# Kernel optimization log

Measured on AMD Instinct MI355X. Metric: run time of the kernel, lower is better.

The kernel has to match this reference:

```python
import jax, jax.numpy as jnp
import numpy as np
import math

B, S, D, H = 2, 2048, 1024, 16
DK = D // H

def setup_inputs() -> dict:
    key = jax.random.key(0)
    ks = jax.random.split(key, 12)
    def xavier(k, shape):
        fan_in, fan_out = shape[1], shape[0]
        limit = math.sqrt(6.0 / (fan_in + fan_out))
        return jax.random.uniform(k, shape, jnp.float32, -limit, limit)
    inp = {
        'query': jax.random.normal(ks[0], (B, S, D), jnp.float32),
        'key':   jax.random.normal(ks[1], (B, S, D), jnp.float32),
        'value': jax.random.normal(ks[2], (B, S, D), jnp.float32),
        # causal mask, broadcast over heads: (B, 1, S, S), 1 = keep, 0 = mask
        'mask':  jnp.broadcast_to(jnp.tril(jnp.ones((S, S), jnp.int32)), (B, 1, S, S)),
        'Wq': xavier(ks[3], (D, D)), 'bq': jnp.zeros((D,), jnp.float32),
        'Wk': xavier(ks[4], (D, D)), 'bk': jnp.zeros((D,), jnp.float32),
        'Wv': xavier(ks[5], (D, D)), 'bv': jnp.zeros((D,), jnp.float32),
        'Wo': xavier(ks[6], (D, D)), 'bo': jnp.zeros((D,), jnp.float32),
    }
    return inp

def _split_heads(x):
    # (B, S, D) -> (B, H, S, DK)
    b, s, _ = x.shape
    return x.reshape(b, s, H, DK).transpose(0, 2, 1, 3)

def reference(query, key, value, mask, Wq, bq, Wk, bk, Wv, bv, Wo, bo):
    # torch nn.Linear: y = x @ W.T + b
    Q = _split_heads(query @ Wq.T + bq)   # (B,H,S,DK)
    K = _split_heads(key   @ Wk.T + bk)
    V = _split_heads(value @ Wv.T + bv)
    scores = jnp.einsum('bhqd,bhkd->bhqk', Q, K) / math.sqrt(DK)  # (B,H,S,S)
    scores = jnp.where(mask == 0, jnp.float32(-1e9), scores)
    attn = jax.nn.softmax(scores, axis=-1)  # dropout p=0 -> identity
    out = jnp.einsum('bhqk,bhkd->bhqd', attn, V)  # (B,H,S,DK)
    out = out.transpose(0, 2, 1, 3).reshape(query.shape[0], query.shape[1], D)
    return out @ Wo.T + bo
```

## Files before the change

### kernel.cpp

```cpp
#include <hip/hip_runtime.h>
#include <hip/hip_bf16.h>
#include <type_traits>


typedef __attribute__((ext_vector_type(8))) short short8;
typedef __attribute__((ext_vector_type(4))) short s16x4;
typedef __attribute__((ext_vector_type(4))) float floatx4;

__device__ __forceinline__ short f2bf(float x) {
    union { float f; unsigned u; } v; v.f = x;
    unsigned r = v.u + 0x7fffu + ((v.u >> 16) & 1u);
    return (short)(r >> 16);
}

__device__ __forceinline__ unsigned pk2bf(float a, float b) {
    union { __hip_bfloat162 h2; unsigned u; } cv;
    cv.h2 = __float22bfloat162_rn(make_float2(a, b));
    return cv.u;
}

__device__ __forceinline__ float fast_exp2(float x) {
#if __has_builtin(__builtin_amdgcn_exp2f)
    return __builtin_amdgcn_exp2f(x);
#else
    return __expf(x * 0.69314718056f);
#endif
}

typedef __attribute__((address_space(3))) short lds_short;
typedef __attribute__((address_space(1))) const short glb_short;
__device__ __forceinline__ void load_lds16(const void* g, void* l) {
    __builtin_amdgcn_global_load_lds((glb_short*)g, (lds_short*)l, 16, 0, 0);
}

__global__ __launch_bounds__(256) void cvt_all(
        const float* __restrict__ q, const float* __restrict__ k,
        const float* __restrict__ v,
        const float* __restrict__ wq, const float* __restrict__ wk,
        const float* __restrict__ wv, const float* __restrict__ wo,
        unsigned short* __restrict__ xq, unsigned short* __restrict__ xk,
        unsigned short* __restrict__ xv,
        unsigned short* __restrict__ wqb, unsigned short* __restrict__ wkb,
        unsigned short* __restrict__ wvb, unsigned short* __restrict__ wob) {
    const float* s; unsigned short* d;
    int bx = blockIdx.x;
    switch (blockIdx.y) {
        case 0: s = q; d = xq; break;
        case 1: s = k; d = xk; break;
        case 2: s = v; d = xv; break;
        default: {
            int wsel = bx >> 9; bx &= 511;
            s = (wsel == 0) ? wq : (wsel == 1) ? wk : (wsel == 2) ? wv : wo;
            d = (wsel == 0) ? wqb : (wsel == 1) ? wkb : (wsel == 2) ? wvb : wob;
        }
    }
    size_t i = ((size_t)bx * 256 + threadIdx.x) * 8;
    floatx4 a = *(const floatx4*)(s + i), b2 = *(const floatx4*)(s + i + 4);
    union { unsigned u[4]; short8 v8; } o;
    o.u[0] = pk2bf(a[0], a[1]);  o.u[1] = pk2bf(a[2], a[3]);
    o.u[2] = pk2bf(b2[0], b2[1]); o.u[3] = pk2bf(b2[2], b2[3]);
    *(short8*)(d + i) = o.v8;
}

__global__ __launch_bounds__(256) void gemm_qkv(
        const unsigned short* __restrict__ Xq, const unsigned short* __restrict__ Xk,
        const unsigned short* __restrict__ Xv,
        const unsigned short* __restrict__ Wq, const unsigned short* __restrict__ Wk,
        const unsigned short* __restrict__ Wv,
        const float* __restrict__ bq, const float* __restrict__ bk,
        const float* __restrict__ bv,
        unsigned short* __restrict__ Qb, unsigned short* __restrict__ Kb,
        unsigned short* __restrict__ Vb) {
    constexpr int K = 1024, N = 1024;
    __shared__ short As[128 * 64];
    __shared__ short Bs[128 * 64];
    const int t = threadIdx.x;
    const int slot = blockIdx.x;
    const int p = (slot & 7) + 8 * (slot >> 6);
    const int nx = (slot >> 3) & 7;
    const int chunk = p >> 5, my = p & 31;
    const unsigned short* A = chunk == 0 ? Xq : chunk == 1 ? Xk : Xv;
    const unsigned short* W = chunk == 0 ? Wq : chunk == 1 ? Wk : Wv;
    const float* bias        = chunk == 0 ? bq : chunk == 1 ? bk : bv;
    unsigned short* Y        = chunk == 0 ? Qb : chunk == 1 ? Kb : Vb;
    const float scale = chunk == 0 ? 0.1803368801f : 1.0f;
    const int m0 = my * 128, n0 = nx * 128;
    const int lane = t & 63, w = t >> 6;
    const int l16 = lane & 15, quad = lane >> 4;
    const int wm = w >> 1, wn = w & 1;
    const int srow8 = t >> 3, scs8 = t & 7;
    floatx4 acc[4][4] = {};

    for (int k0 = 0; k0 < K; k0 += 64) {
        __syncthreads();
        for (int i = 0; i < 4; i++) {
            const int row = i * 32 + srow8;
            const int cg = scs8 ^ (row & 7);
            load_lds16(A + (size_t)(m0 + row) * K + k0 + cg * 8, &As[i * 2048 + t * 8]);
            load_lds16(W + (size_t)(n0 + row) * K + k0 + cg * 8, &Bs[i * 2048 + t * 8]);
        }
        __syncthreads();

        for (int kc = 0; kc < 2; kc++) {
            short8 af[4], bf[4];
            for (int ms = 0; ms < 4; ms++) {
                const int row = wm * 64 + ms * 16 + l16;
                af[ms] = *(short8*)&As[row * 64 + (((kc << 2) | quad) ^ (row & 7)) * 8];
            }
            for (int ns = 0; ns < 4; ns++) {
                const int row = wn * 64 + ns * 16 + l16;
                bf[ns] = *(short8*)&Bs[row * 64 + (((kc << 2) | quad) ^ (row & 7)) * 8];
            }
            for (int ms = 0; ms < 4; ms++)
                for (int ns = 0; ns < 4; ns++)
                    acc[ms][ns] = __builtin_amdgcn_mfma_f32_16x16x32_bf16(
                            af[ms], bf[ns], acc[ms][ns], 0, 0, 0);
        }
    }

    for (int ms = 0; ms < 4; ms++)
        for (int ns = 0; ns < 4; ns++) {
            int col = n0 + wn * 64 + ns * 16 + l16;
            float bb = bias[col];
            for (int r = 0; r < 4; r++) {
                int row = m0 + wm * 64 + ms * 16 + quad * 4 + r;
                Y[(size_t)row * N + col] =
                    (unsigned short)f2bf((acc[ms][ns][r] + bb) * scale);
            }
        }
}

__global__ __launch_bounds__(256) void gemm_o(
        const unsigned short* __restrict__ A, const unsigned short* __restrict__ W,
        const float* __restrict__ bo, float* __restrict__ out) {
    constexpr int K = 1024, N = 1024;
    __shared__ short As[128 * 64];
    __shared__ short Bs[64 * 64];
    const int t = threadIdx.x;
    const int slot = blockIdx.x;
    const int z = slot >> 6;
    const int pm = (slot & 7) + 8 * (z >> 1);
    const int nx = ((slot >> 3) & 7) + 8 * (z & 1);
    const int m0 = pm * 128, n0 = nx * 64;
    const int lane = t & 63, w = t >> 6;
    const int l16 = lane & 15, quad = lane >> 4;
    const int wm = w >> 1, wn = w & 1;
    const int srow8 = t >> 3, scs8 = t & 7;
    floatx4 acc[4][2] = {};

    for (int k0 = 0; k0 < K; k0 += 64) {
        __syncthreads();
        for (int i = 0; i < 4; i++) {
            const int row = i * 32 + srow8;
            const int cg = scs8 ^ (row & 7);
            load_lds16(A + (size_t)(m0 + row) * K + k0 + cg * 8, &As[i * 2048 + t * 8]);
        }
        for (int i = 0; i < 2; i++) {
            const int row = i * 32 + srow8;
            const int cg = scs8 ^ (row & 7);
            load_lds16(W + (size_t)(n0 + row) * K + k0 + cg * 8, &Bs[i * 2048 + t * 8]);
        }
        __syncthreads();

        for (int kc = 0; kc < 2; kc++) {
            short8 af[4], bf[2];
            for (int ms = 0; ms < 4; ms++) {
                const int row = wm * 64 + ms * 16 + l16;
                af[ms] = *(short8*)&As[row * 64 + (((kc << 2) | quad) ^ (row & 7)) * 8];
            }
            for (int ns = 0; ns < 2; ns++) {
                const int row = wn * 32 + ns * 16 + l16;
                bf[ns] = *(short8*)&Bs[row * 64 + (((kc << 2) | quad) ^ (row & 7)) * 8];
            }
            for (int ms = 0; ms < 4; ms++)
                for (int ns = 0; ns < 2; ns++)
                    acc[ms][ns] = __builtin_amdgcn_mfma_f32_16x16x32_bf16(
                            af[ms], bf[ns], acc[ms][ns], 0, 0, 0);
        }
    }

    for (int ms = 0; ms < 4; ms++)
        for (int ns = 0; ns < 2; ns++) {
            int col = n0 + wn * 32 + ns * 16 + l16;
            float bb = bo[col];
            for (int r = 0; r < 4; r++) {
                int row = m0 + wm * 64 + ms * 16 + quad * 4 + r;
                out[(size_t)row * N + col] = acc[ms][ns][r] + bb;
            }
        }
}

__global__ __launch_bounds__(256) void attn_kernel(
        const unsigned short* __restrict__ Q, const unsigned short* __restrict__ Kp,
        const unsigned short* __restrict__ Vp, unsigned short* __restrict__ O) {
    __shared__ short Ks[64 * 72];
    __shared__ short Vt[64 * 72];
    __shared__ short Ps[8][16 * 72];
    const int t = threadIdx.x;
    const int bx = blockIdx.x;
    const int g = (bx >> 5) & 15, bh = bx & 31;
    const int tile = (bx < 256) ? (15 - g) : (g - 8);
    const int h = bh & 15, b = bh >> 4;
    const int q0 = tile * 128;
    const int lane = t & 63, w = t >> 6, l16 = lane & 15, quad = lane >> 4;
    const int krow = t >> 2, kcg = (t & 3) * 16;
    const int vp2 = t & 31, vg = t >> 5;

    short8 qa[2], qb[2];
    {
        const size_t baseA = ((size_t)(b * 2048 + q0 + w * 32 + l16)) * 1024 + h * 64;
        qa[0] = *(const short8*)(Q + baseA + quad * 8);
        qa[1] = *(const short8*)(Q + baseA + 32 + quad * 8);
        const size_t baseB = baseA + (size_t)16 * 1024;
        qb[0] = *(const short8*)(Q + baseB + quad * 8);
        qb[1] = *(const short8*)(Q + baseB + 32 + quad * 8);
    }
    float lA = 0.f, lB = 0.f;
    floatx4 oA[4] = {}, oB[4] = {};

    short8 ka, kb, va, vc;
    {
        const size_t kbse = ((size_t)(b * 2048 + krow)) * 1024 + h * 64 + kcg;
        ka = *(const short8*)(Kp + kbse);
        kb = *(const short8*)(Kp + kbse + 8);
        const size_t vbse = ((size_t)(b * 2048 + 2 * vp2)) * 1024 + h * 64 + vg * 8;
        va = *(const short8*)(Vp + vbse);
        vc = *(const short8*)(Vp + vbse + 1024);
    }

    const int kv_hi = q0 + 128;
    for (int kv0 = 0; kv0 < kv_hi; kv0 += 64) {
        __syncthreads();
        *(short8*)&Ks[krow * 72 + kcg] = ka;
        *(short8*)&Ks[krow * 72 + kcg + 8] = kb;
        for (int i = 0; i < 8; i++) {
            unsigned pk = (unsigned)(unsigned short)va[i] |
                          ((unsigned)(unsigned short)vc[i] << 16);
            *(unsigned*)&Vt[(vg * 8 + i) * 72 + 2 * vp2] = pk;
        }
        __syncthreads();

        if (kv0 + 64 < kv_hi) {
            const size_t kbse = ((size_t)(b * 2048 + kv0 + 64 + krow)) * 1024 + h * 64 + kcg;
            ka = *(const short8*)(Kp + kbse);
            kb = *(const short8*)(Kp + kbse + 8);
            const size_t vbse = ((size_t)(b * 2048 + kv0 + 64 + 2 * vp2)) * 1024 + h * 64 + vg * 8;
            va = *(const short8*)(Vp + vbse);
            vc = *(const short8*)(Vp + vbse + 1024);
        }

        floatx4 sA[4] = {}, sB[4] = {};
        __builtin_amdgcn_s_setprio(1);
        for (int hh = 0; hh < 4; hh++)
            for (int kc = 0; kc < 2; kc++) {
                short8 kf = *(short8*)&Ks[(hh * 16 + l16) * 72 + kc * 32 + quad * 8];
                sA[hh] = __builtin_amdgcn_mfma_f32_16x16x32_bf16(kf, qa[kc], sA[hh], 0, 0, 0);
                sB[hh] = __builtin_amdgcn_mfma_f32_16x16x32_bf16(kf, qb[kc], sB[hh], 0, 0, 0);
            }
        __builtin_amdgcn_s_setprio(0);

        {
            const bool nm = (kv0 + 63 > q0 + w * 32);
            const int qg = q0 + w * 32 + l16;
            float ls = 0.f;
            for (int hh = 0; hh < 4; hh++) {
                float pv[4];
                for (int r = 0; r < 4; r++) {
                    int kv = kv0 + hh * 16 + quad * 4 + r;
                    float e = fast_exp2(sA[hh][r]);
                    pv[r] = (nm && kv > qg) ? 0.f : e;
                    ls += pv[r];
                }
                union { unsigned u[2]; s16x4 v4; } pw;
                pw.u[0] = pk2bf(pv[0], pv[1]); pw.u[1] = pk2bf(pv[2], pv[3]);
                *(s16x4*)&Ps[2 * w][l16 * 72 + hh * 16 + quad * 4] = pw.v4;
            }
            ls += __shfl_xor(ls, 16);
            ls += __shfl_xor(ls, 32);
            lA += ls;
        }
        {
            const bool nm = (kv0 + 63 > q0 + w * 32 + 16);
            const int qg = q0 + w * 32 + 16 + l16;
            float ls = 0.f;
            for (int hh = 0; hh < 4; hh++) {
                float pv[4];
                for (int r = 0; r < 4; r++) {
                    int kv = kv0 + hh * 16 + quad * 4 + r;
                    float e = fast_exp2(sB[hh][r]);
                    pv[r] = (nm && kv > qg) ? 0.f : e;
                    ls += pv[r];
                }
                union { unsigned u[2]; s16x4 v4; } pw;
                pw.u[0] = pk2bf(pv[0], pv[1]); pw.u[1] = pk2bf(pv[2], pv[3]);
                *(s16x4*)&Ps[2 * w + 1][l16 * 72 + hh * 16 + quad * 4] = pw.v4;
            }
            ls += __shfl_xor(ls, 16);
            ls += __shfl_xor(ls, 32);
            lB += ls;
        }

        short8 pa0 = *(short8*)&Ps[2 * w][l16 * 72 + quad * 8];
        short8 pa1 = *(short8*)&Ps[2 * w][l16 * 72 + 32 + quad * 8];
        short8 pb0 = *(short8*)&Ps[2 * w + 1][l16 * 72 + quad * 8];
        short8 pb1 = *(short8*)&Ps[2 * w + 1][l16 * 72 + 32 + quad * 8];
        __builtin_amdgcn_s_setprio(1);
        for (int nc = 0; nc < 4; nc++) {
            short8 vf0 = *(short8*)&Vt[(nc * 16 + l16) * 72 + quad * 8];
            short8 vf1 = *(short8*)&Vt[(nc * 16 + l16) * 72 + 32 + quad * 8];
            oA[nc] = __builtin_amdgcn_mfma_f32_16x16x32_bf16(vf0, pa0, oA[nc], 0, 0, 0);
            oA[nc] = __builtin_amdgcn_mfma_f32_16x16x32_bf16(vf1, pa1, oA[nc], 0, 0, 0);
            oB[nc] = __builtin_amdgcn_mfma_f32_16x16x32_bf16(vf0, pb0, oB[nc], 0, 0, 0);
            oB[nc] = __builtin_amdgcn_mfma_f32_16x16x32_bf16(vf1, pb1, oB[nc], 0, 0, 0);
        }
        __builtin_amdgcn_s_setprio(0);
    }

    {
        const float rl = 1.f / lA;
        const size_t orow = ((size_t)(b * 2048 + q0 + w * 32 + l16)) * 1024 + h * 64;
        for (int nc = 0; nc < 4; nc++) {
            union { unsigned u[2]; s16x4 v4; } ow;
            ow.u[0] = pk2bf(oA[nc][0] * rl, oA[nc][1] * rl);
            ow.u[1] = pk2bf(oA[nc][2] * rl, oA[nc][3] * rl);
            *(s16x4*)(O + orow + nc * 16 + quad * 4) = ow.v4;
        }
    }
    {
        const float rl = 1.f / lB;
        const size_t orow = ((size_t)(b * 2048 + q0 + w * 32 + 16 + l16)) * 1024 + h * 64;
        for (int nc = 0; nc < 4; nc++) {
            union { unsigned u[2]; s16x4 v4; } ow;
            ow.u[0] = pk2bf(oB[nc][0] * rl, oB[nc][1] * rl);
            ow.u[1] = pk2bf(oB[nc][2] * rl, oB[nc][3] * rl);
            *(s16x4*)(O + orow + nc * 16 + quad * 4) = ow.v4;
        }
    }
}

extern "C" void kernel_launch(void* const* d_in, const int* in_sizes, int n_in,
                              void* d_out, int out_size, void* d_ws, size_t ws_size,
                              hipStream_t stream) {
    const float* query = (const float*)d_in[0];
    const float* key   = (const float*)d_in[1];
    const float* value = (const float*)d_in[2];
    const float* Wq = (const float*)d_in[4];
    const float* bq = (const float*)d_in[5];
    const float* Wk = (const float*)d_in[6];
    const float* bk = (const float*)d_in[7];
    const float* Wv = (const float*)d_in[8];
    const float* bv = (const float*)d_in[9];
    const float* Wo = (const float*)d_in[10];
    const float* bo = (const float*)d_in[11];

    const size_t NE = (size_t)4096 * 1024;
    const size_t WE = (size_t)1024 * 1024;
    unsigned short* Xq  = (unsigned short*)d_ws;
    unsigned short* Xk  = Xq + NE;
    unsigned short* Xv  = Xk + NE;
    unsigned short* Qb  = Xv + NE;
    unsigned short* Kb  = Qb + NE;
    unsigned short* Vb  = Kb + NE;
    unsigned short* Ob  = Vb + NE;
    unsigned short* Wqb = Ob + NE;
    unsigned short* Wkb = Wqb + WE;
    unsigned short* Wvb = Wkb + WE;
    unsigned short* Wob = Wvb + WE;

    cvt_all<<<dim3(2048, 4), 256, 0, stream>>>(query, key, value, Wq, Wk, Wv, Wo,
                                               Xq, Xk, Xv, Wqb, Wkb, Wvb, Wob);
    gemm_qkv<<<dim3(768), 256, 0, stream>>>(Xq, Xk, Xv, Wqb, Wkb, Wvb,
                                            bq, bk, bv, Qb, Kb, Vb);
    attn_kernel<<<dim3(512), 256, 0, stream>>>(Qb, Kb, Vb, Ob);
    gemm_o<<<dim3(512), 256, 0, stream>>>(Ob, Wob, bo, (float*)d_out);
}
```

Baseline: 245.4 us.

## Halve attention query tile to 64 rows with 128-thread blocks and rebalanced scheduling

The attention kernel now uses 64-row query tiles per block, launched as 1024 blocks of 128 threads (two waves) instead of 512 blocks of 256. Each thread stages twice as much K/V data per iteration to fill the shared tiles. Block indices are remapped so long causal tiles are scheduled first and paired with short ones, improving load balance and occupancy. The cost is that each K/V tile is loaded by twice as many blocks, and per-thread global load work grows.

```diff
diff --git a/kernel.cpp b/kernel.cpp
--- a/kernel.cpp
+++ b/kernel.cpp
@@ -190,20 +190,22 @@
         }
 }
 
-__global__ __launch_bounds__(256) void attn_kernel(
+__global__ __launch_bounds__(128) void attn_kernel(
         const unsigned short* __restrict__ Q, const unsigned short* __restrict__ Kp,
         const unsigned short* __restrict__ Vp, unsigned short* __restrict__ O) {
     __shared__ short Ks[64 * 72];
     __shared__ short Vt[64 * 72];
-    __shared__ short Ps[8][16 * 72];
+    __shared__ short Ps[4][16 * 72];
     const int t = threadIdx.x;
     const int bx = blockIdx.x;
-    const int g = (bx >> 5) & 15, bh = bx & 31;
-    const int tile = (bx < 256) ? (15 - g) : (g - 8);
+    const int g = bx >> 8, c = bx & 255;
+    const int dlt = c >> 5, bh = c & 31;
+    const int unit = (g == 0) ? 31 - dlt : (g == 1) ? 23 - dlt
+                   : (g == 2) ? 8 + dlt  : dlt;
     const int h = bh & 15, b = bh >> 4;
-    const int q0 = tile * 128;
+    const int q0 = unit * 64;
     const int lane = t & 63, w = t >> 6, l16 = lane & 15, quad = lane >> 4;
-    const int krow = t >> 2, kcg = (t & 3) * 16;
+    const int krow = t >> 1, kcg = (t & 1) * 32;
     const int vp2 = t & 31, vg = t >> 5;
 
     short8 qa[2], qb[2];
@@ -218,35 +220,47 @@
     float lA = 0.f, lB = 0.f;
     floatx4 oA[4] = {}, oB[4] = {};
 
-    short8 ka, kb, va, vc;
+    short8 ka, kb, kc_, kd, va, vb, vc, vd;
     {
         const size_t kbse = ((size_t)(b * 2048 + krow)) * 1024 + h * 64 + kcg;
-        ka = *(const short8*)(Kp + kbse);
-        kb = *(const short8*)(Kp + kbse + 8);
+        ka  = *(const short8*)(Kp + kbse);
+        kb  = *(const short8*)(Kp + kbse + 8);
+        kc_ = *(const short8*)(Kp + kbse + 16);
+        kd  = *(const short8*)(Kp + kbse + 24);
         const size_t vbse = ((size_t)(b * 2048 + 2 * vp2)) * 1024 + h * 64 + vg * 8;
         va = *(const short8*)(Vp + vbse);
         vc = *(const short8*)(Vp + vbse + 1024);
-    }
-
-    const int kv_hi = q0 + 128;
-    for (int kv0 = 0; kv0 < kv_hi; kv0 += 64) {
-        __syncthreads();
-        *(short8*)&Ks[krow * 72 + kcg] = ka;
-        *(short8*)&Ks[krow * 72 + kcg + 8] = kb;
+        vb = *(const short8*)(Vp + vbse + 32);
+        vd = *(const short8*)(Vp + vbse + 1024 + 32);
+    }
+
+    for (int kv0 = 0; kv0 <= q0; kv0 += 64) {
+        __syncthreads();
+        *(short8*)&Ks[krow * 72 + kcg]      = ka;
+        *(short8*)&Ks[krow * 72 + kcg + 8]  = kb;
+        *(short8*)&Ks[krow * 72 + kcg + 16] = kc_;
+        *(short8*)&Ks[krow * 72 + kcg + 24] = kd;
         for (int i = 0; i < 8; i++) {
-            unsigned pk = (unsigned)(unsigned short)va[i] |
+            unsigned p0 = (unsigned)(unsigned short)va[i] |
                           ((unsigned)(unsigned short)vc[i] << 16);
-            *(unsigned*)&Vt[(vg * 8 + i) * 72 + 2 * vp2] = pk;
-        }
-        __syncthreads();
-
-        if (kv0 + 64 < kv_hi) {
+            *(unsigned*)&Vt[(vg * 8 + i) * 72 + 2 * vp2] = p0;
+            unsigned p1 = (unsigned)(unsigned short)vb[i] |
+                          ((unsigned)(unsigned short)vd[i] << 16);
+            *(unsigned*)&Vt[(vg * 8 + i + 32) * 72 + 2 * vp2] = p1;
+        }
+        __syncthreads();
+
+        if (kv0 < q0) {
             const size_t kbse = ((size_t)(b * 2048 + kv0 + 64 + krow)) * 1024 + h * 64 + kcg;
-            ka = *(const short8*)(Kp + kbse);
-            kb = *(const short8*)(Kp + kbse + 8);
+            ka  = *(const short8*)(Kp + kbse);
+            kb  = *(const short8*)(Kp + kbse + 8);
+            kc_ = *(const short8*)(Kp + kbse + 16);
+            kd  = *(const short8*)(Kp + kbse + 24);
             const size_t vbse = ((size_t)(b * 2048 + kv0 + 64 + 2 * vp2)) * 1024 + h * 64 + vg * 8;
             va = *(const short8*)(Vp + vbse);
             vc = *(const short8*)(Vp + vbse + 1024);
+            vb = *(const short8*)(Vp + vbse + 32);
+            vd = *(const short8*)(Vp + vbse + 1024 + 32);
         }
 
         floatx4 sA[4] = {}, sB[4] = {};
@@ -371,6 +385,6 @@
                                                Xq, Xk, Xv, Wqb, Wkb, Wvb, Wob);
     gemm_qkv<<<dim3(768), 256, 0, stream>>>(Xq, Xk, Xv, Wqb, Wkb, Wvb,
                                             bq, bk, bv, Qb, Kb, Vb);
-    attn_kernel<<<dim3(512), 256, 0, stream>>>(Qb, Kb, Vb, Ob);
+    attn_kernel<<<dim3(1024), 128, 0, stream>>>(Qb, Kb, Vb, Ob);
     gemm_o<<<dim3(512), 256, 0, stream>>>(Ob, Wob, bo, (float*)d_out);
 }
```

New measurement: 246.2 us. Within noise of the previous version (+0.4%).
